# Optimization experiments

Hardware: AMD Instinct MI355X
Metric: run time of the kernel (lower is better)

The kernel has to match this reference:

```python
import jax, jax.numpy as jnp
import numpy as np

DIM = 768
N_HEADS = 12
HEAD_DIM = DIM // N_HEADS
HIDDEN = 4 * DIM
B, T = 16, 577
EPS = 1e-6


def _layer_norm(x, w, b):
    mu = jnp.mean(x, axis=-1, keepdims=True)
    var = jnp.mean(jnp.square(x - mu), axis=-1, keepdims=True)
    return (x - mu) * jax.lax.rsqrt(var + EPS) * w + b


def setup_inputs() -> dict:
    key = jax.random.key(0)
    ks = jax.random.split(key, 8)
    s = lambda fan_in: 1.0 / np.sqrt(fan_in)
    return {
        "x": jax.random.normal(ks[0], (B, T, DIM), jnp.float32),
        "ln1_w": jnp.ones((DIM,), jnp.float32),
        "ln1_b": jnp.zeros((DIM,), jnp.float32),
        "qkv_w": jax.random.normal(ks[1], (DIM, 3 * DIM), jnp.float32) * s(DIM),
        "qkv_b": jnp.zeros((3 * DIM,), jnp.float32),
        "proj_w": jax.random.normal(ks[2], (DIM, DIM), jnp.float32) * s(DIM),
        "proj_b": jnp.zeros((DIM,), jnp.float32),
        "ln2_w": jnp.ones((DIM,), jnp.float32),
        "ln2_b": jnp.zeros((DIM,), jnp.float32),
        "fc1_w": jax.random.normal(ks[3], (DIM, HIDDEN), jnp.float32) * s(DIM),
        "fc1_b": jnp.zeros((HIDDEN,), jnp.float32),
        "fc2_w": jax.random.normal(ks[4], (HIDDEN, DIM), jnp.float32) * s(HIDDEN),
        "fc2_b": jnp.zeros((DIM,), jnp.float32),
    }


def reference(x, ln1_w, ln1_b, qkv_w, qkv_b, proj_w, proj_b,
              ln2_w, ln2_b, fc1_w, fc1_b, fc2_w, fc2_b):
    # --- attention branch ---
    h = _layer_norm(x, ln1_w, ln1_b)                      # [B,T,D]
    qkv = h @ qkv_w + qkv_b                               # [B,T,3D]
    qkv = qkv.reshape(B, T, 3, N_HEADS, HEAD_DIM)
    q, k, v = jnp.moveaxis(qkv, 2, 0)                     # each [B,T,H,hd]
    scale = HEAD_DIM ** -0.5
    dp = jnp.einsum('bqhd,bkhd->bhqk', q, k) * scale      # [B,H,T,T]
    attn = jax.nn.softmax(dp, axis=-1)
    wa = jnp.einsum('bhqk,bkhd->bqhd', attn, v)           # [B,T,H,hd]
    wa = wa.reshape(B, T, DIM)
    x = x + wa @ proj_w + proj_b
    # --- MLP branch ---
    h = _layer_norm(x, ln2_w, ln2_b)
    h = jax.nn.gelu(h @ fc1_w + fc1_b, approximate=False)
    x = x + h @ fc2_w + fc2_b
    return x
```

## Files before the change

kernel.cpp:

```cpp
#include <hip/hip_runtime.h>
#include <math.h>

#define DIM 768
#define NH 12
#define HIDDEN 3072
#define BB 16
#define TT 577
#define TPAD 640
#define BT (BB*TT)
#define MPAD 9344

typedef _Float16 f16x8 __attribute__((ext_vector_type(8)));
typedef __attribute__((ext_vector_type(4))) float f32x4;

__global__ __launch_bounds__(256) void ln_kernel(const float* __restrict__ x,
                                                 const float* __restrict__ w,
                                                 const float* __restrict__ b,
                                                 _Float16* __restrict__ oh) {
    int row = blockIdx.x;
    const float* xr = x + (size_t)row * DIM;
    int t = threadIdx.x;
    float v0 = xr[t], v1 = xr[t + 256], v2 = xr[t + 512];
    float s = v0 + v1 + v2;
    float sq = v0 * v0 + v1 * v1 + v2 * v2;
    __shared__ float red[8];
    int lane = t & 63, wid = t >> 6;
    #pragma unroll
    for (int off = 32; off; off >>= 1) {
        s  += __shfl_down(s, off);
        sq += __shfl_down(sq, off);
    }
    if (lane == 0) { red[wid] = s; red[4 + wid] = sq; }
    __syncthreads();
    if (t == 0) {
        float ts = red[0] + red[1] + red[2] + red[3];
        float tq = red[4] + red[5] + red[6] + red[7];
        float mu = ts * (1.0f / DIM);
        float var = tq * (1.0f / DIM) - mu * mu;
        red[0] = mu;
        red[1] = rsqrtf(var + 1e-6f);
    }
    __syncthreads();
    float mu = red[0], rstd = red[1];
    int sw = (row & 7) << 3;
    size_t ro = (size_t)row * DIM;
    #pragma unroll
    for (int e = 0; e < 3; ++e) {
        int c = t + e * 256;
        float v = (e == 0 ? v0 : (e == 1 ? v1 : v2));
        float val = (v - mu) * rstd * w[c] + b[c];
        oh[ro + (c ^ sw)] = (_Float16)val;
    }
}

__global__ __launch_bounds__(256) void convert_wT(const float* __restrict__ src,
                                                  _Float16* __restrict__ dh,
                                                  int K, int N) {
    int n = blockIdx.x * 64 + (threadIdx.x & 63);
    int k0 = blockIdx.y * 32 + (threadIdx.x >> 6) * 8;
    f16x8 h8;
    #pragma unroll
    for (int j = 0; j < 8; ++j) h8[j] = (_Float16)src[(size_t)(k0 + j) * N + n];
    *(f16x8*)&dh[(size_t)n * K + (k0 ^ ((n & 7) << 3))] = h8;
}

template<int EPI>
__global__ __launch_bounds__(256) void gemm_mfma(
    const _Float16* __restrict__ A, const _Float16* __restrict__ B,
    const float* __restrict__ bias, const float* __restrict__ resid,
    float* __restrict__ C, _Float16* __restrict__ O,
    _Float16* __restrict__ pQ, _Float16* __restrict__ pK, _Float16* __restrict__ pVT,
    int M, int N, int K) {
    __shared__ _Float16 lds[2][2][128][64];
    int tid = threadIdx.x;
    int wid = tid >> 6, lane = tid & 63;
    int m0 = blockIdx.y * 128, n0 = blockIdx.x * 128;
    int wr = wid >> 1, wc = wid & 1;

    const _Float16* src = (wid < 2) ? A : B;
    int srow0 = ((wid < 2) ? m0 : n0) + (wid & 1) * 64;
    const _Float16* gbase = src + (size_t)(srow0 + (lane >> 3)) * K + (lane & 7) * 8;
    _Float16* lb[2] = { &lds[0][wid >> 1][(wid & 1) * 64][0],
                        &lds[1][wid >> 1][(wid & 1) * 64][0] };

    f32x4 acc[4][4];
    #pragma unroll
    for (int i = 0; i < 4; ++i)
        #pragma unroll
        for (int j = 0; j < 4; ++j) acc[i][j] = (f32x4)0.0f;

    const int nk = K >> 6;
    #pragma unroll
    for (int i = 0; i < 8; ++i)
        __builtin_amdgcn_global_load_lds(
            (const __attribute__((address_space(1))) void*)(gbase + (size_t)i * 8 * K),
            (__attribute__((address_space(3))) void*)(lb[0] + i * 512), 16, 0, 0);
    __syncthreads();

    int cur = 0;
    for (int ks = 0; ks < nk; ++ks) {
        if (ks + 1 < nk) {
            int k0 = (ks + 1) << 6;
            #pragma unroll
            for (int i = 0; i < 8; ++i)
                __builtin_amdgcn_global_load_lds(
                    (const __attribute__((address_space(1))) void*)(gbase + (size_t)i * 8 * K + k0),
                    (__attribute__((address_space(3))) void*)(lb[cur ^ 1] + i * 512), 16, 0, 0);
        }
        #pragma unroll
        for (int kk = 0; kk < 2; ++kk) {
            int so = (((kk * 4 + (lane >> 4)) ^ (lane & 7)) << 3);
            f16x8 af[4], bf[4];
            #pragma unroll
            for (int m = 0; m < 4; ++m)
                af[m] = *(const f16x8*)&lds[cur][0][wr * 64 + m * 16 + (lane & 15)][so];
            #pragma unroll
            for (int n = 0; n < 4; ++n)
                bf[n] = *(const f16x8*)&lds[cur][1][wc * 64 + n * 16 + (lane & 15)][so];
            #pragma unroll
            for (int m = 0; m < 4; ++m)
                #pragma unroll
                for (int n = 0; n < 4; ++n)
                    acc[m][n] = __builtin_amdgcn_mfma_f32_16x16x32_f16(af[m], bf[n], acc[m][n], 0, 0, 0);
        }
        __syncthreads();
        cur ^= 1;
    }

    int rbase = m0 + wr * 64 + (lane >> 4) * 4;
    int cbase = n0 + wc * 64 + (lane & 15);
    #pragma unroll
    for (int mi = 0; mi < 4; ++mi) {
        #pragma unroll
        for (int ni = 0; ni < 4; ++ni) {
            int c = cbase + ni * 16;
            float bsv = bias[c];
            #pragma unroll
            for (int r4 = 0; r4 < 4; ++r4) {
                int r = rbase + mi * 16 + r4;
                if (r >= M) continue;
                float v = acc[mi][ni][r4] + bsv;
                if (EPI == 1) {
                    v = v / (1.0f + __expf(-1.5957691216f * (v + 0.044715f * v * v * v)));
                    O[(size_t)r * N + (c ^ ((r & 7) << 3))] = (_Float16)v;
                } else if (EPI == 2) {
                    v += resid[(size_t)r * N + c];
                    C[(size_t)r * N + c] = v;
                } else {
                    int b_ = r / TT, t_ = r - b_ * TT;
                    int which = c / DIM, cc = c - which * DIM;
                    int head = cc >> 6, d = cc & 63;
                    size_t bh = (size_t)b_ * NH + head;
                    if (which == 0) {
                        pQ[(bh * TPAD + t_) * 64 + d] = (_Float16)(v * 0.125f);
                    } else if (which == 1) {
                        pK[(bh * TPAD + t_) * 64 + (d ^ ((t_ & 7) << 3))] = (_Float16)v;
                    } else {
                        pVT[(bh * 64 + d) * TPAD + ((t_ & ~63) | ((t_ & 63) ^ ((d & 7) << 3)))] = (_Float16)v;
                    }
                }
            }
        }
    }
}

__global__ __launch_bounds__(256) void attn_mfma(
    const _Float16* __restrict__ Q, const _Float16* __restrict__ Kp,
    const _Float16* __restrict__ VT, _Float16* __restrict__ wa) {
    __shared__ _Float16 lds[20480];
    int tid = threadIdx.x, wid = tid >> 6, lane = tid & 63;
    int qt = blockIdx.x, h = blockIdx.y, b = blockIdx.z;
    size_t bh = (size_t)b * NH + h;

    int qrow = qt * 64 + wid * 16 + (lane & 15);
    const _Float16* qb = Q + (bh * TPAD + qrow) * 64 + (lane >> 4) * 8;
    f16x8 qf[2];
    qf[0] = *(const f16x8*)qb;
    qf[1] = *(const f16x8*)(qb + 32);

    f32x4 oacc[4];
    #pragma unroll
    for (int dt = 0; dt < 4; ++dt) oacc[dt] = (f32x4)0.0f;
    float m[4] = {-1e30f, -1e30f, -1e30f, -1e30f};
    float lsum[4] = {0.f, 0.f, 0.f, 0.f};

    _Float16* pbase = &lds[16384 + wid * 1024];
    const _Float16* gK = Kp + (bh * TPAD + (wid & 1) * 32 + (lane >> 3)) * 64 + (lane & 7) * 8;
    const _Float16* gV = VT + (bh * 64 + (wid & 1) * 32 + (lane >> 3)) * TPAD + (lane & 7) * 8;
    int dstoff = (wid >> 1) * 4096 + (wid & 1) * 2048;

    #pragma unroll
    for (int i = 0; i < 4; ++i) {
        const _Float16* g = (wid < 2) ? (gK + (size_t)i * 8 * 64) : (gV + (size_t)i * 8 * TPAD);
        __builtin_amdgcn_global_load_lds(
            (const __attribute__((address_space(1))) void*)g,
            (__attribute__((address_space(3))) void*)(&lds[dstoff] + i * 512), 16, 0, 0);
    }
    __syncthreads();

    int cur = 0;
    for (int kt0 = 0; kt0 < TT; kt0 += 64) {
        if (kt0 + 64 < TT) {
            int nxt = kt0 + 64;
            #pragma unroll
            for (int i = 0; i < 4; ++i) {
                const _Float16* g = (wid < 2) ? (gK + (size_t)(nxt) * 64 + (size_t)i * 8 * 64)
                                              : (gV + nxt + (size_t)i * 8 * TPAD);
                __builtin_amdgcn_global_load_lds(
                    (const __attribute__((address_space(1))) void*)g,
                    (__attribute__((address_space(3))) void*)(&lds[(cur ^ 1) * 8192 + dstoff] + i * 512),
                    16, 0, 0);
            }
        }
        const _Float16* kbuf = &lds[cur * 8192];
        const _Float16* vbuf = &lds[cur * 8192 + 4096];

        f32x4 sacc[4];
        #pragma unroll
        for (int kt = 0; kt < 4; ++kt) sacc[kt] = (f32x4)0.0f;
        #pragma unroll
        for (int dstep = 0; dstep < 2; ++dstep) {
            #pragma unroll
            for (int kt = 0; kt < 4; ++kt) {
                int krow = kt * 16 + (lane & 15);
                int ko = (((dstep * 4 + (lane >> 4)) ^ (krow & 7)) << 3);
                f16x8 kb = *(const f16x8*)&kbuf[krow * 64 + ko];
                sacc[kt] = __builtin_amdgcn_mfma_f32_16x16x32_f16(qf[dstep], kb, sacc[kt], 0, 0, 0);
            }
        }
        #pragma unroll
        for (int kt = 0; kt < 4; ++kt) {
            int kcol = kt0 + kt * 16 + (lane & 15);
            if (kcol >= TT) {
                #pragma unroll
                for (int r = 0; r < 4; ++r) sacc[kt][r] = -1e30f;
            }
        }
        float mt[4];
        #pragma unroll
        for (int r = 0; r < 4; ++r)
            mt[r] = fmaxf(fmaxf(sacc[0][r], sacc[1][r]), fmaxf(sacc[2][r], sacc[3][r]));
        #pragma unroll
        for (int off = 1; off <= 8; off <<= 1) {
            #pragma unroll
            for (int r = 0; r < 4; ++r) mt[r] = fmaxf(mt[r], __shfl_xor(mt[r], off));
        }
        float corr[4];
        #pragma unroll
        for (int r = 0; r < 4; ++r) {
            float nm = fmaxf(m[r], mt[r]);
            corr[r] = __expf(m[r] - nm);
            m[r] = nm;
        }
        float rowsum[4] = {0.f, 0.f, 0.f, 0.f};
        #pragma unroll
        for (int kt = 0; kt < 4; ++kt) {
            #pragma unroll
            for (int r = 0; r < 4; ++r) {
                float p = __expf(sacc[kt][r] - m[r]);
                rowsum[r] += p;
                int q = (lane >> 4) * 4 + r;
                int kcol = kt * 16 + (lane & 15);
                pbase[q * 64 + (kcol ^ ((q & 7) << 3))] = (_Float16)p;
            }
        }
        #pragma unroll
        for (int off = 1; off <= 8; off <<= 1) {
            #pragma unroll
            for (int r = 0; r < 4; ++r) rowsum[r] += __shfl_xor(rowsum[r], off);
        }
        #pragma unroll
        for (int r = 0; r < 4; ++r) {
            lsum[r] = lsum[r] * corr[r] + rowsum[r];
            #pragma unroll
            for (int dt = 0; dt < 4; ++dt) oacc[dt][r] *= corr[r];
        }
        #pragma unroll
        for (int kc = 0; kc < 2; ++kc) {
            int q = lane & 15;
            int pko = (((kc * 4 + (lane >> 4)) ^ (q & 7)) << 3);
            f16x8 pa = *(const f16x8*)&pbase[q * 64 + pko];
            #pragma unroll
            for (int dt = 0; dt < 4; ++dt) {
                int drow = dt * 16 + (lane & 15);
                int vo = (((kc * 4 + (lane >> 4)) ^ (drow & 7)) << 3);
                f16x8 vb = *(const f16x8*)&vbuf[drow * 64 + vo];
                oacc[dt] = __builtin_amdgcn_mfma_f32_16x16x32_f16(pa, vb, oacc[dt], 0, 0, 0);
            }
        }
        __syncthreads();
        cur ^= 1;
    }

    #pragma unroll
    for (int r = 0; r < 4; ++r) {
        int t = qt * 64 + wid * 16 + (lane >> 4) * 4 + r;
        if (t >= TT) continue;
        float inv = 1.0f / lsum[r];
        size_t row = (size_t)b * TT + t;
        int sw = (int)(row & 7) << 3;
        size_t ro = row * DIM;
        #pragma unroll
        for (int dt = 0; dt < 4; ++dt) {
            int c = h * 64 + dt * 16 + (lane & 15);
            wa[ro + (c ^ sw)] = (_Float16)(oacc[dt][r] * inv);
        }
    }
}

extern "C" void kernel_launch(void* const* d_in, const int* in_sizes, int n_in,
                              void* d_out, int out_size, void* d_ws, size_t ws_size,
                              hipStream_t stream) {
    const float* x      = (const float*)d_in[0];
    const float* ln1_w  = (const float*)d_in[1];
    const float* ln1_b  = (const float*)d_in[2];
    const float* qkv_w  = (const float*)d_in[3];
    const float* qkv_b  = (const float*)d_in[4];
    const float* proj_w = (const float*)d_in[5];
    const float* proj_b = (const float*)d_in[6];
    const float* ln2_w  = (const float*)d_in[7];
    const float* ln2_b  = (const float*)d_in[8];
    const float* fc1_w  = (const float*)d_in[9];
    const float* fc1_b  = (const float*)d_in[10];
    const float* fc2_w  = (const float*)d_in[11];
    const float* fc2_b  = (const float*)d_in[12];
    float* out = (float*)d_out;

    const size_t P768  = (size_t)MPAD * 768;
    const size_t P3072 = (size_t)MPAD * 3072;
    const size_t PQKV  = (size_t)BB * NH * TPAD * 64;
    char* wsb = (char*)d_ws;
    auto alloc = [&](size_t bytes) -> char* {
        char* p = wsb;
        wsb += (bytes + 255) & ~(size_t)255;
        return p;
    };
    _Float16* h_p   = (_Float16*)alloc(P768 * 2);
    _Float16* wa_p  = (_Float16*)alloc(P768 * 2);
    float* x1 = (float*)alloc((size_t)BT * 768 * 4);
    _Float16* qkvT = (_Float16*)alloc((size_t)2304 * 768 * 2);
    _Float16* projT = (_Float16*)alloc((size_t)768 * 768 * 2);
    _Float16* fc1T = (_Float16*)alloc((size_t)3072 * 768 * 2);
    _Float16* fc2T = (_Float16*)alloc((size_t)768 * 3072 * 2);
    char* ubase = alloc(P3072 * 2 > 3 * PQKV * 2 ? P3072 * 2 : 3 * PQKV * 2);
    _Float16* pQ  = (_Float16*)ubase;
    _Float16* pK  = pQ + PQKV;
    _Float16* pVT = pK + PQKV;
    _Float16* hh  = (_Float16*)ubase;

    dim3 blk(256);
    int mt = (BT + 127) / 128;

    convert_wT<<<dim3(2304 / 64, 768 / 32), blk, 0, stream>>>(qkv_w, qkvT, 768, 2304);
    convert_wT<<<dim3(768 / 64, 768 / 32), blk, 0, stream>>>(proj_w, projT, 768, 768);
    convert_wT<<<dim3(3072 / 64, 768 / 32), blk, 0, stream>>>(fc1_w, fc1T, 768, 3072);
    convert_wT<<<dim3(768 / 64, 3072 / 32), blk, 0, stream>>>(fc2_w, fc2T, 3072, 768);

    ln_kernel<<<BT, blk, 0, stream>>>(x, ln1_w, ln1_b, h_p);
    gemm_mfma<3><<<dim3(2304 / 128, mt), blk, 0, stream>>>(h_p, qkvT, qkv_b,
        nullptr, nullptr, nullptr, pQ, pK, pVT, BT, 2304, 768);
    attn_mfma<<<dim3((TT + 63) / 64, NH, BB), blk, 0, stream>>>(pQ, pK, pVT, wa_p);
    gemm_mfma<2><<<dim3(768 / 128, mt), blk, 0, stream>>>(wa_p, projT, proj_b,
        x, x1, nullptr, nullptr, nullptr, nullptr, BT, 768, 768);
    ln_kernel<<<BT, blk, 0, stream>>>(x1, ln2_w, ln2_b, h_p);
    gemm_mfma<1><<<dim3(3072 / 128, mt), blk, 0, stream>>>(h_p, fc1T, fc1_b,
        nullptr, nullptr, hh, nullptr, nullptr, nullptr, BT, 3072, 768);
    gemm_mfma<2><<<dim3(768 / 128, mt), blk, 0, stream>>>(hh, fc2T, fc2_b,
        x1, out, nullptr, nullptr, nullptr, nullptr, BT, 768, 3072);
}
```

Baseline: 490.0 us.

## Remap GEMM workgroups per XCD and stage GELU epilogue through LDS for vector stores

Workgroup IDs in the GEMM are remapped so that consecutive tiles land on the same XCD (hardware IDs interleave round-robin across 8 XCDs), which should improve L2 reuse of the A/B tiles. The fc1 GELU epilogue now writes fp16 results into LDS, then emits 16-byte vectorized global stores per row instead of scattered 2-byte stores. The attention-kernel variable renames only avoid a name clash. The risks are extra integer index math, an added barrier and LDS round trip in the epilogue, and an LDS tile of 128x136 halves that fits inside the existing buffer.

```diff
diff --git a/kernel.cpp b/kernel.cpp
--- a/kernel.cpp
+++ b/kernel.cpp
@@ -74,7 +74,16 @@
     __shared__ _Float16 lds[2][2][128][64];
     int tid = threadIdx.x;
     int wid = tid >> 6, lane = tid & 63;
-    int m0 = blockIdx.y * 128, n0 = blockIdx.x * 128;
+
+    int gx = gridDim.x;
+    int nwg = gx * gridDim.y;
+    int hw = blockIdx.y * gx + blockIdx.x;
+    int xcd = hw & 7, loc = hw >> 3;
+    int q = nwg >> 3, r = nwg & 7;
+    int wg = (xcd < r ? xcd * (q + 1) : r * (q + 1) + (xcd - r) * q) + loc;
+    int bxl = wg % gx, byl = wg / gx;
+
+    int m0 = byl * 128, n0 = bxl * 128;
     int wr = wid >> 1, wc = wid & 1;
 
     const _Float16* src = (wid < 2) ? A : B;
@@ -127,6 +136,41 @@
         cur ^= 1;
     }
 
+    if (EPI == 1) {
+        _Float16* eb = &lds[0][0][0][0];
+        int rl0 = wr * 64 + (lane >> 4) * 4;
+        int cl0 = wc * 64 + (lane & 15);
+        #pragma unroll
+        for (int mi = 0; mi < 4; ++mi) {
+            #pragma unroll
+            for (int ni = 0; ni < 4; ++ni) {
+                int cl = cl0 + ni * 16;
+                float bsv = bias[n0 + cl];
+                #pragma unroll
+                for (int r4 = 0; r4 < 4; ++r4) {
+                    int rl = rl0 + mi * 16 + r4;
+                    float v = acc[mi][ni][r4] + bsv;
+                    v = v / (1.0f + __expf(-1.5957691216f * (v + 0.044715f * v * v * v)));
+                    eb[rl * 136 + cl] = (_Float16)v;
+                }
+            }
+        }
+        __syncthreads();
+        int rl = tid >> 1;
+        int rowg = m0 + rl;
+        if (rowg < M) {
+            int sw = (rowg & 7) << 3;
+            int c0 = (tid & 1) * 64;
+            size_t rb = (size_t)rowg * N;
+            #pragma unroll
+            for (int j = 0; j < 8; ++j) {
+                f16x8 v = *(const f16x8*)&eb[rl * 136 + c0 + j * 8];
+                *(f16x8*)&O[rb + ((n0 + c0 + j * 8) ^ sw)] = v;
+            }
+        }
+        return;
+    }
+
     int rbase = m0 + wr * 64 + (lane >> 4) * 4;
     int cbase = n0 + wc * 64 + (lane & 15);
     #pragma unroll
@@ -140,10 +184,7 @@
                 int r = rbase + mi * 16 + r4;
                 if (r >= M) continue;
                 float v = acc[mi][ni][r4] + bsv;
-                if (EPI == 1) {
-                    v = v / (1.0f + __expf(-1.5957691216f * (v + 0.044715f * v * v * v)));
-                    O[(size_t)r * N + (c ^ ((r & 7) << 3))] = (_Float16)v;
-                } else if (EPI == 2) {
+                if (EPI == 2) {
                     v += resid[(size_t)r * N + c];
                     C[(size_t)r * N + c] = v;
                 } else {
@@ -259,9 +300,9 @@
             for (int r = 0; r < 4; ++r) {
                 float p = __expf(sacc[kt][r] - m[r]);
                 rowsum[r] += p;
-                int q = (lane >> 4) * 4 + r;
+                int qq = (lane >> 4) * 4 + r;
                 int kcol = kt * 16 + (lane & 15);
-                pbase[q * 64 + (kcol ^ ((q & 7) << 3))] = (_Float16)p;
+                pbase[qq * 64 + (kcol ^ ((qq & 7) << 3))] = (_Float16)p;
             }
         }
         #pragma unroll
@@ -277,9 +318,9 @@
         }
         #pragma unroll
         for (int kc = 0; kc < 2; ++kc) {
-            int q = lane & 15;
-            int pko = (((kc * 4 + (lane >> 4)) ^ (q & 7)) << 3);
-            f16x8 pa = *(const f16x8*)&pbase[q * 64 + pko];
+            int qq = lane & 15;
+            int pko = (((kc * 4 + (lane >> 4)) ^ (qq & 7)) << 3);
+            f16x8 pa = *(const f16x8*)&pbase[qq * 64 + pko];
             #pragma unroll
             for (int dt = 0; dt < 4; ++dt) {
                 int drow = dt * 16 + (lane & 15);
```

Result: faster. 475.7 us (-2.9%).
